# Performance work log

Hardware: AMD Instinct MI355X
Metric: run time of the kernel (lower is better)

## Reference

```python
import jax, jax.numpy as jnp
import numpy as np

N = 100000
E = 1600000
F_IN = 16
HEADS = 4
OUT_CH = 32  # conv_filters[i] // heads = 128 // 4
HID = HEADS * OUT_CH  # 128
N_GRAPHS = 64
N_TARGETS = 4
EPS_BN = 1e-5


def setup_inputs() -> dict:
    key = jax.random.key(0)
    ks = jax.random.split(key, 32)
    glorot = lambda k, shp: jax.random.normal(k, shp, jnp.float32) * np.sqrt(2.0 / (shp[0] + shp[-1]))
    inp = {
        "node_features": jax.random.normal(ks[0], (N, F_IN), jnp.float32),
        "edge_index": jax.random.randint(ks[1], (2, E), 0, N, jnp.int64),
        "batch": jnp.sort(jax.random.randint(ks[2], (N,), 0, N_GRAPHS, jnp.int64)),
        # GAT layer 1: F_IN -> HEADS*OUT_CH
        "W1": glorot(ks[3], (F_IN, HID)),
        "b1": jnp.zeros((HID,), jnp.float32),
        "att_src1": glorot(ks[4], (HEADS, OUT_CH)),
        "att_dst1": glorot(ks[5], (HEADS, OUT_CH)),
        "bn_g1": jnp.ones((HID,), jnp.float32),
        "bn_b1": jnp.zeros((HID,), jnp.float32),
        # GAT layer 2: HID -> HID
        "W2": glorot(ks[6], (HID, HID)),
        "b2": jnp.zeros((HID,), jnp.float32),
        "att_src2": glorot(ks[7], (HEADS, OUT_CH)),
        "att_dst2": glorot(ks[8], (HEADS, OUT_CH)),
        "bn_g2": jnp.ones((HID,), jnp.float32),
        "bn_b2": jnp.zeros((HID,), jnp.float32),
        # dense head 128 -> 64 -> 32 -> 4
        "d1_W": glorot(ks[9], (HID, HID // 2)),
        "d1_b": jnp.zeros((HID // 2,), jnp.float32),
        "bn_g_d1": jnp.ones((HID // 2,), jnp.float32),
        "bn_b_d1": jnp.zeros((HID // 2,), jnp.float32),
        "d2_W": glorot(ks[10], (HID // 2, HID // 4)),
        "d2_b": jnp.zeros((HID // 4,), jnp.float32),
        "bn_g_d2": jnp.ones((HID // 4,), jnp.float32),
        "bn_b_d2": jnp.zeros((HID // 4,), jnp.float32),
        "fc_W": glorot(ks[11], (HID // 4, N_TARGETS)),
        "fc_b": jnp.zeros((N_TARGETS,), jnp.float32),
    }
    return inp


def batch_norm(x, gamma, beta):
    # training-mode BatchNorm1d: biased batch stats over dim 0
    mu = jnp.mean(x, axis=0)
    var = jnp.mean(jnp.square(x - mu), axis=0)
    return gamma * (x - mu) * jax.lax.rsqrt(var + EPS_BN) + beta


def gat_conv(x, src, dst, W, b, att_src, att_dst):
    # PyG GATConv (shared lin, concat heads): h = x @ W -> [N, H, C]
    h = (x @ W).reshape(-1, HEADS, OUT_CH)
    a_s = jnp.sum(h * att_src, axis=-1)  # [N, H]
    a_d = jnp.sum(h * att_dst, axis=-1)  # [N, H]
    e = jax.nn.leaky_relu(a_s[src] + a_d[dst], 0.2)  # [E, H]
    # softmax over incoming edges per destination node
    m = jax.ops.segment_max(e, dst, num_segments=N)
    m = jnp.where(jnp.isfinite(m), m, 0.0)
    w = jnp.exp(e - m[dst])
    s = jax.ops.segment_sum(w, dst, num_segments=N)
    alpha = w / (s[dst] + 1e-16)  # [E, H]
    out = jax.ops.segment_sum(h[src] * alpha[:, :, None], dst, num_segments=N)
    return out.reshape(-1, HID) + b


def reference(node_features, edge_index, batch,
              W1, b1, att_src1, att_dst1, bn_g1, bn_b1,
              W2, b2, att_src2, att_dst2, bn_g2, bn_b2,
              d1_W, d1_b, bn_g_d1, bn_b_d1,
              d2_W, d2_b, bn_g_d2, bn_b_d2,
              fc_W, fc_b):
    src, dst = edge_index[0], edge_index[1]
    x = gat_conv(node_features, src, dst, W1, b1, att_src1, att_dst1)
    x = jax.nn.relu(batch_norm(x, bn_g1, bn_b1))
    x = gat_conv(x, src, dst, W2, b2, att_src2, att_dst2)
    x = jax.nn.relu(batch_norm(x, bn_g2, bn_b2))
    # global mean pool over graphs
    sums = jax.ops.segment_sum(x, batch, num_segments=N_GRAPHS)
    cnt = jax.ops.segment_sum(jnp.ones((x.shape[0],), x.dtype), batch, num_segments=N_GRAPHS)
    g = sums / jnp.maximum(cnt, 1.0)[:, None]  # [G, HID]
    g = jax.nn.relu(batch_norm(g @ d1_W + d1_b, bn_g_d1, bn_b_d1))
    g = jax.nn.relu(batch_norm(g @ d2_W + d2_b, bn_g_d2, bn_b_d2))
    return g @ fc_W + fc_b
```

## Files before the change

kernel.cpp:

```cpp
#include <hip/hip_runtime.h>

#define HID 128
#define NG 64

__device__ __forceinline__ float lrelu(float v) { return v > 0.0f ? v : 0.2f * v; }

__device__ __forceinline__ unsigned int bf16rne(float f) {
    unsigned int u = __float_as_uint(f);
    return (u + 0x7fffu + ((u >> 16) & 1u)) >> 16;
}
__device__ __forceinline__ unsigned int packbf(float a, float b) {
    return bf16rne(a) | (bf16rne(b) << 16);
}

template <int K, bool BN>
__global__ __launch_bounds__(256) void k_gemm(const float* __restrict__ xin,
        const float* __restrict__ W,
        const float* __restrict__ scale, const float* __restrict__ shift,
        const float* __restrict__ attS, const float* __restrict__ attD,
        unsigned short* __restrict__ h, float* __restrict__ as_, float* __restrict__ ad_, int N)
{
    __shared__ float xs[64][K];
    constexpr int K4 = K / 4;
    int t = threadIdx.x;
    int cq = t & 31;
    int nr = t >> 5;

    float4 atS = ((const float4*)attS)[cq];
    float4 atD = ((const float4*)attD)[cq];

    for (int n0 = blockIdx.x * 64; n0 < N; n0 += gridDim.x * 64) {
        int nrem = N - n0; if (nrem > 64) nrem = 64;
        for (int idx = t; idx < 64 * K4; idx += 256) {
            int n = idx / K4, k4 = idx % K4;
            float4 v = make_float4(0.f, 0.f, 0.f, 0.f);
            if (n < nrem) {
                v = ((const float4*)(xin + (size_t)(n0 + n) * K))[k4];
                if (BN) {
                    float4 sc = ((const float4*)scale)[k4];
                    float4 sh = ((const float4*)shift)[k4];
                    v.x = fmaf(v.x, sc.x, sh.x); v.x = v.x > 0.f ? v.x : 0.f;
                    v.y = fmaf(v.y, sc.y, sh.y); v.y = v.y > 0.f ? v.y : 0.f;
                    v.z = fmaf(v.z, sc.z, sh.z); v.z = v.z > 0.f ? v.z : 0.f;
                    v.w = fmaf(v.w, sc.w, sh.w); v.w = v.w > 0.f ? v.w : 0.f;
                }
            }
            *(float4*)(&xs[n][k4 * 4]) = v;
        }
        __syncthreads();

        float4 acc[8];
#pragma unroll
        for (int j = 0; j < 8; ++j) acc[j] = make_float4(0.f, 0.f, 0.f, 0.f);

        const float4* W4 = (const float4*)W;
#pragma unroll 2
        for (int k4 = 0; k4 < K4; ++k4) {
            float4 w0 = W4[(k4 * 4 + 0) * 32 + cq];
            float4 w1 = W4[(k4 * 4 + 1) * 32 + cq];
            float4 w2 = W4[(k4 * 4 + 2) * 32 + cq];
            float4 w3 = W4[(k4 * 4 + 3) * 32 + cq];
#pragma unroll
            for (int j = 0; j < 8; ++j) {
                float4 xv = *(const float4*)(&xs[nr * 8 + j][k4 * 4]);
                acc[j].x = fmaf(xv.x, w0.x, acc[j].x);
                acc[j].y = fmaf(xv.x, w0.y, acc[j].y);
                acc[j].z = fmaf(xv.x, w0.z, acc[j].z);
                acc[j].w = fmaf(xv.x, w0.w, acc[j].w);
                acc[j].x = fmaf(xv.y, w1.x, acc[j].x);
                acc[j].y = fmaf(xv.y, w1.y, acc[j].y);
                acc[j].z = fmaf(xv.y, w1.z, acc[j].z);
                acc[j].w = fmaf(xv.y, w1.w, acc[j].w);
                acc[j].x = fmaf(xv.z, w2.x, acc[j].x);
                acc[j].y = fmaf(xv.z, w2.y, acc[j].y);
                acc[j].z = fmaf(xv.z, w2.z, acc[j].z);
                acc[j].w = fmaf(xv.z, w2.w, acc[j].w);
                acc[j].x = fmaf(xv.w, w3.x, acc[j].x);
                acc[j].y = fmaf(xv.w, w3.y, acc[j].y);
                acc[j].z = fmaf(xv.w, w3.z, acc[j].z);
                acc[j].w = fmaf(xv.w, w3.w, acc[j].w);
            }
        }

#pragma unroll
        for (int j = 0; j < 8; ++j) {
            int n = nr * 8 + j;
            bool ok = (n < nrem);
            if (ok) {
                unsigned int lo = packbf(acc[j].x, acc[j].y);
                unsigned int hi = packbf(acc[j].z, acc[j].w);
                ((uint2*)(h + (size_t)(n0 + n) * 128))[cq] = make_uint2(lo, hi);
            }
            float ps = acc[j].x * atS.x + acc[j].y * atS.y + acc[j].z * atS.z + acc[j].w * atS.w;
            float pd = acc[j].x * atD.x + acc[j].y * atD.y + acc[j].z * atD.z + acc[j].w * atD.w;
            ps += __shfl_xor(ps, 1); pd += __shfl_xor(pd, 1);
            ps += __shfl_xor(ps, 2); pd += __shfl_xor(pd, 2);
            ps += __shfl_xor(ps, 4); pd += __shfl_xor(pd, 4);
            if (ok && (cq & 7) == 0) {
                int hd = cq >> 3;
                as_[(size_t)(n0 + n) * 4 + hd] = ps;
                ad_[(size_t)(n0 + n) * 4 + hd] = pd;
            }
        }
        __syncthreads();
    }
}

__global__ __launch_bounds__(256) void k_bhist(const int* __restrict__ ei,
        int* __restrict__ bSize, int E, int nB)
{
    __shared__ int hist[1024];
    int t = threadIdx.x;
    for (int i = t; i < nB; i += 256) hist[i] = 0;
    __syncthreads();
    int chunk = (E + gridDim.x - 1) / gridDim.x;
    int lo = blockIdx.x * chunk, hi = lo + chunk; if (hi > E) hi = E;
    for (int e = lo + t; e < hi; e += 256) atomicAdd(&hist[ei[E + e] >> 8], 1);
    __syncthreads();
    for (int i = t; i < nB; i += 256) { int c = hist[i]; if (c) atomicAdd(&bSize[i], c); }
}

__global__ __launch_bounds__(512) void k_bscan(const int* __restrict__ bSize,
        int* __restrict__ bOff, int* __restrict__ bCur, int nB)
{
    __shared__ int part[512];
    int t = threadIdx.x;
    part[t] = (t < nB) ? bSize[t] : 0;
    __syncthreads();
    for (int off = 1; off < 512; off <<= 1) {
        int u = (t >= off) ? part[t - off] : 0;
        __syncthreads();
        part[t] += u;
        __syncthreads();
    }
    int ex = (t == 0) ? 0 : part[t - 1];
    if (t < nB) { bOff[t] = ex; bCur[t] = ex; }
    if (t == nB - 1) bOff[nB] = part[t];
}

__global__ __launch_bounds__(256) void k_part(const int* __restrict__ ei,
        int* __restrict__ bCur, unsigned long long* __restrict__ bucketBuf, int E, int nB)
{
    __shared__ int hist[1024];
    __shared__ int base[1024];
    int t = threadIdx.x;
    int chunk = (E + gridDim.x - 1) / gridDim.x;
    int lo = blockIdx.x * chunk, hi = lo + chunk; if (hi > E) hi = E;
    for (int i = t; i < nB; i += 256) hist[i] = 0;
    __syncthreads();
    for (int e = lo + t; e < hi; e += 256) atomicAdd(&hist[ei[E + e] >> 8], 1);
    __syncthreads();
    for (int i = t; i < nB; i += 256) {
        int c = hist[i];
        base[i] = c ? atomicAdd(&bCur[i], c) : 0;
        hist[i] = 0;
    }
    __syncthreads();
    for (int e = lo + t; e < hi; e += 256) {
        int s = ei[e], d = ei[E + e];
        int b = d >> 8;
        int pos = base[b] + atomicAdd(&hist[b], 1);
        bucketBuf[pos] = ((unsigned long long)(unsigned)d << 32) | (unsigned)s;
    }
}

__global__ __launch_bounds__(256) void k_build(const unsigned long long* __restrict__ bucketBuf,
        const int* __restrict__ bOff, int* __restrict__ rowPtr, int* __restrict__ sSrc, int N)
{
    __shared__ int lhist[256];
    __shared__ int sOut[8192];
    int b = blockIdx.x;
    int dlo = b << 8;
    int dhi = dlo + 256; if (dhi > N) dhi = N;
    int base = bOff[b], end = bOff[b + 1];
    int sz = end - base;
    int t = threadIdx.x;
    lhist[t] = 0;
    __syncthreads();
    for (int i = t; i < sz; i += 256) {
        int d = (int)(bucketBuf[base + i] >> 32);
        atomicAdd(&lhist[d - dlo], 1);
    }
    __syncthreads();
    for (int off = 1; off < 256; off <<= 1) {
        int u = (t >= off) ? lhist[t - off] : 0;
        __syncthreads();
        lhist[t] += u;
        __syncthreads();
    }
    int pfx = (t == 0) ? 0 : lhist[t - 1];
    if (dlo + t < dhi) rowPtr[dlo + t] = base + pfx;
    if (t == 0 && dhi == N) rowPtr[N] = end;
    __syncthreads();
    lhist[t] = pfx;
    __syncthreads();
    if (sz <= 8192) {
        for (int i = t; i < sz; i += 256) {
            unsigned long long p = bucketBuf[base + i];
            int d = (int)(p >> 32), s = (int)(p & 0xffffffffu);
            int pos = atomicAdd(&lhist[d - dlo], 1);
            sOut[pos] = s;
        }
        __syncthreads();
        for (int i = t; i < sz; i += 256) sSrc[base + i] = sOut[i];
    } else {
        for (int i = t; i < sz; i += 256) {
            unsigned long long p = bucketBuf[base + i];
            int d = (int)(p >> 32), s = (int)(p & 0xffffffffu);
            int pos = atomicAdd(&lhist[d - dlo], 1);
            sSrc[base + pos] = s;
        }
    }
}

__global__ __launch_bounds__(256) void k_alpha(const int* __restrict__ rowPtr,
        const int* __restrict__ sSrc,
        const float* __restrict__ as_, const float* __restrict__ ad_,
        float* __restrict__ alpha, float* __restrict__ sums, int N)
{
    int t = threadIdx.x;
    int lane8 = t & 7;
    int d = blockIdx.x * 32 + (t >> 3);
    if (d >= N) return;
    int b0 = rowPtr[d], b1 = rowPtr[d + 1];
    float4 adv = ((const float4*)ad_)[d];

    float4 m = make_float4(-3.4e38f, -3.4e38f, -3.4e38f, -3.4e38f);
    for (int j = b0 + lane8; j < b1; j += 8) {
        int s = sSrc[j];
        float4 a = ((const float4*)as_)[s];
        m.x = fmaxf(m.x, lrelu(a.x + adv.x));
        m.y = fmaxf(m.y, lrelu(a.y + adv.y));
        m.z = fmaxf(m.z, lrelu(a.z + adv.z));
        m.w = fmaxf(m.w, lrelu(a.w + adv.w));
    }
#pragma unroll
    for (int off = 1; off < 8; off <<= 1) {
        m.x = fmaxf(m.x, __shfl_xor(m.x, off));
        m.y = fmaxf(m.y, __shfl_xor(m.y, off));
        m.z = fmaxf(m.z, __shfl_xor(m.z, off));
        m.w = fmaxf(m.w, __shfl_xor(m.w, off));
    }
    float4 sum = make_float4(0.f, 0.f, 0.f, 0.f);
    for (int j = b0 + lane8; j < b1; j += 8) {
        int s = sSrc[j];
        float4 a = ((const float4*)as_)[s];
        float4 w;
        w.x = __expf(lrelu(a.x + adv.x) - m.x);
        w.y = __expf(lrelu(a.y + adv.y) - m.y);
        w.z = __expf(lrelu(a.z + adv.z) - m.z);
        w.w = __expf(lrelu(a.w + adv.w) - m.w);
        ((float4*)alpha)[j] = w;
        sum.x += w.x; sum.y += w.y; sum.z += w.z; sum.w += w.w;
    }
#pragma unroll
    for (int off = 1; off < 8; off <<= 1) {
        sum.x += __shfl_xor(sum.x, off);
        sum.y += __shfl_xor(sum.y, off);
        sum.z += __shfl_xor(sum.z, off);
        sum.w += __shfl_xor(sum.w, off);
    }
    if (lane8 == 0) ((float4*)sums)[d] = sum;
}

__global__ __launch_bounds__(256) void k_agg(const int* __restrict__ rowPtr,
        const int* __restrict__ sSrc,
        const float* __restrict__ alpha, const float* __restrict__ sums,
        const unsigned short* __restrict__ h, float* __restrict__ out, int N)
{
    int t = threadIdx.x;
    int lane = t & 31;
    int d = blockIdx.x * 8 + (t >> 5);
    if (d >= N) return;
    int hd = lane >> 3;
    int b0 = rowPtr[d], b1 = rowPtr[d + 1];
    const uint2* h2 = (const uint2*)h;

    float4 acc = make_float4(0.f, 0.f, 0.f, 0.f);
    int j = b0;
    for (; j + 4 <= b1; j += 4) {
        int s0 = sSrc[j], s1 = sSrc[j + 1], s2 = sSrc[j + 2], s3 = sSrc[j + 3];
        float w0 = alpha[(size_t)j * 4 + hd];
        float w1 = alpha[(size_t)(j + 1) * 4 + hd];
        float w2 = alpha[(size_t)(j + 2) * 4 + hd];
        float w3 = alpha[(size_t)(j + 3) * 4 + hd];
        uint2 u0 = h2[(size_t)s0 * 32 + lane];
        uint2 u1 = h2[(size_t)s1 * 32 + lane];
        uint2 u2 = h2[(size_t)s2 * 32 + lane];
        uint2 u3 = h2[(size_t)s3 * 32 + lane];
        acc.x = fmaf(w0, __uint_as_float(u0.x << 16), acc.x);
        acc.y = fmaf(w0, __uint_as_float(u0.x & 0xffff0000u), acc.y);
        acc.z = fmaf(w0, __uint_as_float(u0.y << 16), acc.z);
        acc.w = fmaf(w0, __uint_as_float(u0.y & 0xffff0000u), acc.w);
        acc.x = fmaf(w1, __uint_as_float(u1.x << 16), acc.x);
        acc.y = fmaf(w1, __uint_as_float(u1.x & 0xffff0000u), acc.y);
        acc.z = fmaf(w1, __uint_as_float(u1.y << 16), acc.z);
        acc.w = fmaf(w1, __uint_as_float(u1.y & 0xffff0000u), acc.w);
        acc.x = fmaf(w2, __uint_as_float(u2.x << 16), acc.x);
        acc.y = fmaf(w2, __uint_as_float(u2.x & 0xffff0000u), acc.y);
        acc.z = fmaf(w2, __uint_as_float(u2.y << 16), acc.z);
        acc.w = fmaf(w2, __uint_as_float(u2.y & 0xffff0000u), acc.w);
        acc.x = fmaf(w3, __uint_as_float(u3.x << 16), acc.x);
        acc.y = fmaf(w3, __uint_as_float(u3.x & 0xffff0000u), acc.y);
        acc.z = fmaf(w3, __uint_as_float(u3.y << 16), acc.z);
        acc.w = fmaf(w3, __uint_as_float(u3.y & 0xffff0000u), acc.w);
    }
    for (; j < b1; ++j) {
        int s = sSrc[j];
        float w = alpha[(size_t)j * 4 + hd];
        uint2 u = h2[(size_t)s * 32 + lane];
        acc.x = fmaf(w, __uint_as_float(u.x << 16), acc.x);
        acc.y = fmaf(w, __uint_as_float(u.x & 0xffff0000u), acc.y);
        acc.z = fmaf(w, __uint_as_float(u.y << 16), acc.z);
        acc.w = fmaf(w, __uint_as_float(u.y & 0xffff0000u), acc.w);
    }
    float inv = 1.f / (sums[(size_t)d * 4 + hd] + 1e-16f);
    acc.x *= inv; acc.y *= inv; acc.z *= inv; acc.w *= inv;
    ((float4*)out)[(size_t)d * 32 + lane] = acc;
}

__global__ __launch_bounds__(256) void k_bnstats(const float* __restrict__ x,
        double* __restrict__ sums, int N)
{
    __shared__ float r1[256], r2[256];
    int t = threadIdx.x;
    int c = t & 127;
    int half = t >> 7;
    float s1 = 0.f, s2 = 0.f;
    for (int n = blockIdx.x * 2 + half; n < N; n += gridDim.x * 2) {
        float v = x[(size_t)n * 128 + c];
        s1 += v; s2 += v * v;
    }
    r1[t] = s1; r2[t] = s2;
    __syncthreads();
    if (t < 128) {
        s1 = r1[t] + r1[t + 128];
        s2 = r2[t] + r2[t + 128];
        atomicAdd(&sums[t], (double)s1);
        atomicAdd(&sums[128 + t], (double)s2);
    }
}

__global__ __launch_bounds__(128) void k_bnscale(const double* __restrict__ sums,
        const float* __restrict__ gamma, const float* __restrict__ beta,
        float* __restrict__ scale, float* __restrict__ shift, int N)
{
    int c = threadIdx.x;
    double mu = sums[c] / (double)N;
    double var = sums[128 + c] / (double)N - mu * mu;
    if (var < 0.0) var = 0.0;
    double rs = 1.0 / sqrt(var + 1e-5);
    float sc = (float)((double)gamma[c] * rs);
    scale[c] = sc;
    shift[c] = beta[c] - (float)mu * sc;
}

__global__ __launch_bounds__(128) void k_pool(const float* __restrict__ x,
        const int* __restrict__ batch, const float* __restrict__ scale, const float* __restrict__ shift,
        float* __restrict__ gsum, float* __restrict__ gcnt, int N)
{
    int lane = threadIdx.x & 31;
    int r = threadIdx.x >> 5;
    int n0 = blockIdx.x * 64;
    if (n0 >= N) return;
    int n1 = n0 + 64; if (n1 > N) n1 = N;
    float4 sc = ((const float4*)scale)[lane];
    float4 sh = ((const float4*)shift)[lane];
    float4 acc = make_float4(0.f, 0.f, 0.f, 0.f);
    int cnt = 0, cur = -1;
    for (int n = n0 + r; n < n1; n += 4) {
        int g = batch[n];
        if (g != cur) {
            if (cur >= 0) {
                atomicAdd(&gsum[cur * 128 + lane * 4 + 0], acc.x);
                atomicAdd(&gsum[cur * 128 + lane * 4 + 1], acc.y);
                atomicAdd(&gsum[cur * 128 + lane * 4 + 2], acc.z);
                atomicAdd(&gsum[cur * 128 + lane * 4 + 3], acc.w);
                if (lane == 0) atomicAdd(&gcnt[cur], (float)cnt);
            }
            acc = make_float4(0.f, 0.f, 0.f, 0.f); cnt = 0; cur = g;
        }
        float4 v = ((const float4*)x)[(size_t)n * 32 + lane];
        v.x = fmaf(v.x, sc.x, sh.x); v.x = v.x > 0.f ? v.x : 0.f;
        v.y = fmaf(v.y, sc.y, sh.y); v.y = v.y > 0.f ? v.y : 0.f;
        v.z = fmaf(v.z, sc.z, sh.z); v.z = v.z > 0.f ? v.z : 0.f;
        v.w = fmaf(v.w, sc.w, sh.w); v.w = v.w > 0.f ? v.w : 0.f;
        acc.x += v.x; acc.y += v.y; acc.z += v.z; acc.w += v.w;
        cnt++;
    }
    if (cur >= 0) {
        atomicAdd(&gsum[cur * 128 + lane * 4 + 0], acc.x);
        atomicAdd(&gsum[cur * 128 + lane * 4 + 1], acc.y);
        atomicAdd(&gsum[cur * 128 + lane * 4 + 2], acc.z);
        atomicAdd(&gsum[cur * 128 + lane * 4 + 3], acc.w);
        if (lane == 0) atomicAdd(&gcnt[cur], (float)cnt);
    }
}

__global__ __launch_bounds__(256) void k_head(const float* __restrict__ gsum, const float* __restrict__ gcnt,
        const float* __restrict__ d1W, const float* __restrict__ d1b,
        const float* __restrict__ g_d1, const float* __restrict__ b_d1,
        const float* __restrict__ d2W, const float* __restrict__ d2b,
        const float* __restrict__ g_d2, const float* __restrict__ b_d2,
        const float* __restrict__ fcW, const float* __restrict__ fcb,
        float* __restrict__ out)
{
    __shared__ float G[64 * 128];
    __shared__ float Y1[64 * 64];
    __shared__ float Y2[64 * 32];
    int t = threadIdx.x;
    for (int i = t; i < 64 * 128; i += 256) {
        int g = i >> 7;
        float cv = gcnt[g]; if (cv < 1.f) cv = 1.f;
        G[i] = gsum[i] / cv;
    }
    __syncthreads();
    for (int i = t; i < 64 * 64; i += 256) {
        int r = i >> 6, j = i & 63;
        float a = 0.f;
        for (int k = 0; k < 128; ++k) a = fmaf(G[r * 128 + k], d1W[k * 64 + j], a);
        Y1[i] = a + d1b[j];
    }
    __syncthreads();
    if (t < 64) {
        float s1 = 0.f, s2 = 0.f;
        for (int r = 0; r < 64; ++r) { float v = Y1[r * 64 + t]; s1 += v; s2 += v * v; }
        float mu = s1 / 64.f, var = s2 / 64.f - mu * mu; if (var < 0.f) var = 0.f;
        float rs = 1.0f / sqrtf(var + 1e-5f);
        float scv = g_d1[t] * rs, shv = b_d1[t] - mu * scv;
        for (int r = 0; r < 64; ++r) {
            float v = fmaf(Y1[r * 64 + t], scv, shv);
            Y1[r * 64 + t] = v > 0.f ? v : 0.f;
        }
    }
    __syncthreads();
    for (int i = t; i < 64 * 32; i += 256) {
        int r = i >> 5, j = i & 31;
        float a = 0.f;
        for (int k = 0; k < 64; ++k) a = fmaf(Y1[r * 64 + k], d2W[k * 32 + j], a);
        Y2[i] = a + d2b[j];
    }
    __syncthreads();
    if (t < 32) {
        float s1 = 0.f, s2 = 0.f;
        for (int r = 0; r < 64; ++r) { float v = Y2[r * 32 + t]; s1 += v; s2 += v * v; }
        float mu = s1 / 64.f, var = s2 / 64.f - mu * mu; if (var < 0.f) var = 0.f;
        float rs = 1.0f / sqrtf(var + 1e-5f);
        float scv = g_d2[t] * rs, shv = b_d2[t] - mu * scv;
        for (int r = 0; r < 64; ++r) {
            float v = fmaf(Y2[r * 32 + t], scv, shv);
            Y2[r * 32 + t] = v > 0.f ? v : 0.f;
        }
    }
    __syncthreads();
    {
        int r = t >> 2, j = t & 3;
        float a = 0.f;
        for (int k = 0; k < 32; ++k) a = fmaf(Y2[r * 32 + k], fcW[k * 4 + j], a);
        out[t] = a + fcb[j];
    }
}

extern "C" void kernel_launch(void* const* d_in, const int* in_sizes, int n_in,
                              void* d_out, int out_size, void* d_ws, size_t ws_size,
                              hipStream_t stream) {
    const int N = in_sizes[0] / 16;
    const int E = in_sizes[1] / 2;
    const int nB = (N + 255) >> 8;

    const float* x        = (const float*)d_in[0];
    const int*   ei       = (const int*)d_in[1];
    const int*   batch    = (const int*)d_in[2];
    const float* W1       = (const float*)d_in[3];
    const float* att_s1   = (const float*)d_in[5];
    const float* att_d1   = (const float*)d_in[6];
    const float* bn_g1    = (const float*)d_in[7];
    const float* bn_b1    = (const float*)d_in[8];
    const float* W2       = (const float*)d_in[9];
    const float* att_s2   = (const float*)d_in[11];
    const float* att_d2   = (const float*)d_in[12];
    const float* bn_g2    = (const float*)d_in[13];
    const float* bn_b2    = (const float*)d_in[14];
    const float* d1W      = (const float*)d_in[15];
    const float* d1b      = (const float*)d_in[16];
    const float* g_d1     = (const float*)d_in[17];
    const float* b_d1     = (const float*)d_in[18];
    const float* d2W      = (const float*)d_in[19];
    const float* d2b      = (const float*)d_in[20];
    const float* g_d2     = (const float*)d_in[21];
    const float* b_d2     = (const float*)d_in[22];
    const float* fcW      = (const float*)d_in[23];
    const float* fcb      = (const float*)d_in[24];
    float* out = (float*)d_out;

    float* ws = (float*)d_ws;
    size_t o = 0;
    unsigned short* hbuf = (unsigned short*)(ws + o); o += (size_t)N * 64;
    float* outb   = ws + o;  o += (size_t)N * 128;
    float* as_    = ws + o;  o += (size_t)N * 4;
    float* ad_    = ws + o;  o += (size_t)N * 4;
    float* alpha  = ws + o;  o += (size_t)E * 4;
    float* sums   = ws + o;  o += (size_t)N * 4;
    float* scale1 = ws + o;  o += 128;
    float* shift1 = ws + o;  o += 128;
    float* scale2 = ws + o;  o += 128;
    float* shift2 = ws + o;  o += 128;
    size_t zoff = o;
    double* bnsum = (double*)(ws + o); o += 512;
    float* gsum   = ws + o;  o += 64 * 128;
    float* gcnt   = ws + o;  o += 64;
    int*   bSize  = (int*)(ws + o); o += 1024;
    size_t zbytes = (o - zoff) * 4;
    int* rowPtr   = (int*)(ws + o); o += (size_t)N + 1;
    int* sSrc     = (int*)(ws + o); o += E;
    int* bOff     = (int*)(ws + o); o += 1025;
    int* bCur     = (int*)(ws + o); o += 1024;
    o = (o + 1) & ~(size_t)1;
    unsigned long long* bucketBuf = (unsigned long long*)(ws + o); o += (size_t)E * 2;

    hipMemsetAsync(ws + zoff, 0, zbytes, stream);

    k_bhist<<<256, 256, 0, stream>>>(ei, bSize, E, nB);
    k_bscan<<<1, 512, 0, stream>>>(bSize, bOff, bCur, nB);
    k_part<<<256, 256, 0, stream>>>(ei, bCur, bucketBuf, E, nB);
    k_build<<<nB, 256, 0, stream>>>(bucketBuf, bOff, rowPtr, sSrc, N);

    int gemm_grid = (N + 63) / 64;
    int alpha_grid = (N + 31) / 32;
    int agg_grid = (N + 7) / 8;

    k_gemm<16, false><<<gemm_grid, 256, 0, stream>>>(x, W1, nullptr, nullptr,
            att_s1, att_d1, hbuf, as_, ad_, N);
    k_alpha<<<alpha_grid, 256, 0, stream>>>(rowPtr, sSrc, as_, ad_, alpha, sums, N);
    k_agg<<<agg_grid, 256, 0, stream>>>(rowPtr, sSrc, alpha, sums, hbuf, outb, N);
    k_bnstats<<<1024, 256, 0, stream>>>(outb, bnsum, N);
    k_bnscale<<<1, 128, 0, stream>>>(bnsum, bn_g1, bn_b1, scale1, shift1, N);

    hipMemsetAsync((void*)bnsum, 0, 512 * 4, stream);

    k_gemm<128, true><<<gemm_grid, 256, 0, stream>>>(outb, W2, scale1, shift1,
            att_s2, att_d2, hbuf, as_, ad_, N);
    k_alpha<<<alpha_grid, 256, 0, stream>>>(rowPtr, sSrc, as_, ad_, alpha, sums, N);
    k_agg<<<agg_grid, 256, 0, stream>>>(rowPtr, sSrc, alpha, sums, hbuf, outb, N);
    k_bnstats<<<1024, 256, 0, stream>>>(outb, bnsum, N);
    k_bnscale<<<1, 128, 0, stream>>>(bnsum, bn_g2, bn_b2, scale2, shift2, N);

    k_pool<<<(N + 63) / 64, 128, 0, stream>>>(outb, batch, scale2, shift2, gsum, gcnt, N);
    k_head<<<1, 256, 0, stream>>>(gsum, gcnt, d1W, d1b, g_d1, b_d1,
                                  d2W, d2b, g_d2, b_d2, fcW, fcb, out);
}
```

Measured before the change: 567.1 us.

## Fuse softmax into aggregation, pack bucket entries to 32 bits, drop bnsum memset

Removes the separate k_alpha kernel and the E×4 alpha buffer. k_agg now computes the per-head softmax denominator itself and recomputes the edge weights from as_/ad_ on the fly, with no max subtraction. Bucket entries shrink from 64-bit (dst,src) pairs to 32-bit words holding the dst low byte and a 24-bit src, which halves partition traffic. Two bnsum buffers replace the mid-stream memset. The trade-offs are an extra pass over neighbours to gather as_ for the sums, a risk of exp overflow without the max shift, and a src limit of 2^24.

```diff
diff --git a/kernel.cpp b/kernel.cpp
--- a/kernel.cpp
+++ b/kernel.cpp
@@ -139,7 +139,7 @@
 }
 
 __global__ __launch_bounds__(256) void k_part(const int* __restrict__ ei,
-        int* __restrict__ bCur, unsigned long long* __restrict__ bucketBuf, int E, int nB)
+        int* __restrict__ bCur, unsigned int* __restrict__ bucketBuf, int E, int nB)
 {
     __shared__ int hist[1024];
     __shared__ int base[1024];
@@ -160,11 +160,11 @@
         int s = ei[e], d = ei[E + e];
         int b = d >> 8;
         int pos = base[b] + atomicAdd(&hist[b], 1);
-        bucketBuf[pos] = ((unsigned long long)(unsigned)d << 32) | (unsigned)s;
-    }
-}
-
-__global__ __launch_bounds__(256) void k_build(const unsigned long long* __restrict__ bucketBuf,
+        bucketBuf[pos] = ((unsigned)(d & 255) << 24) | (unsigned)s;
+    }
+}
+
+__global__ __launch_bounds__(256) void k_build(const unsigned int* __restrict__ bucketBuf,
         const int* __restrict__ bOff, int* __restrict__ rowPtr, int* __restrict__ sSrc, int N)
 {
     __shared__ int lhist[256];
@@ -178,8 +178,7 @@
     lhist[t] = 0;
     __syncthreads();
     for (int i = t; i < sz; i += 256) {
-        int d = (int)(bucketBuf[base + i] >> 32);
-        atomicAdd(&lhist[d - dlo], 1);
+        atomicAdd(&lhist[bucketBuf[base + i] >> 24], 1);
     }
     __syncthreads();
     for (int off = 1; off < 256; off <<= 1) {
@@ -196,76 +195,24 @@
     __syncthreads();
     if (sz <= 8192) {
         for (int i = t; i < sz; i += 256) {
-            unsigned long long p = bucketBuf[base + i];
-            int d = (int)(p >> 32), s = (int)(p & 0xffffffffu);
-            int pos = atomicAdd(&lhist[d - dlo], 1);
-            sOut[pos] = s;
+            unsigned int p = bucketBuf[base + i];
+            int pos = atomicAdd(&lhist[p >> 24], 1);
+            sOut[pos] = (int)(p & 0xffffffu);
         }
         __syncthreads();
         for (int i = t; i < sz; i += 256) sSrc[base + i] = sOut[i];
     } else {
         for (int i = t; i < sz; i += 256) {
-            unsigned long long p = bucketBuf[base + i];
-            int d = (int)(p >> 32), s = (int)(p & 0xffffffffu);
-            int pos = atomicAdd(&lhist[d - dlo], 1);
-            sSrc[base + pos] = s;
-        }
-    }
-}
-
-__global__ __launch_bounds__(256) void k_alpha(const int* __restrict__ rowPtr,
+            unsigned int p = bucketBuf[base + i];
+            int pos = atomicAdd(&lhist[p >> 24], 1);
+            sSrc[base + pos] = (int)(p & 0xffffffu);
+        }
+    }
+}
+
+__global__ __launch_bounds__(256) void k_agg(const int* __restrict__ rowPtr,
         const int* __restrict__ sSrc,
         const float* __restrict__ as_, const float* __restrict__ ad_,
-        float* __restrict__ alpha, float* __restrict__ sums, int N)
-{
-    int t = threadIdx.x;
-    int lane8 = t & 7;
-    int d = blockIdx.x * 32 + (t >> 3);
-    if (d >= N) return;
-    int b0 = rowPtr[d], b1 = rowPtr[d + 1];
-    float4 adv = ((const float4*)ad_)[d];
-
-    float4 m = make_float4(-3.4e38f, -3.4e38f, -3.4e38f, -3.4e38f);
-    for (int j = b0 + lane8; j < b1; j += 8) {
-        int s = sSrc[j];
-        float4 a = ((const float4*)as_)[s];
-        m.x = fmaxf(m.x, lrelu(a.x + adv.x));
-        m.y = fmaxf(m.y, lrelu(a.y + adv.y));
-        m.z = fmaxf(m.z, lrelu(a.z + adv.z));
-        m.w = fmaxf(m.w, lrelu(a.w + adv.w));
-    }
-#pragma unroll
-    for (int off = 1; off < 8; off <<= 1) {
-        m.x = fmaxf(m.x, __shfl_xor(m.x, off));
-        m.y = fmaxf(m.y, __shfl_xor(m.y, off));
-        m.z = fmaxf(m.z, __shfl_xor(m.z, off));
-        m.w = fmaxf(m.w, __shfl_xor(m.w, off));
-    }
-    float4 sum = make_float4(0.f, 0.f, 0.f, 0.f);
-    for (int j = b0 + lane8; j < b1; j += 8) {
-        int s = sSrc[j];
-        float4 a = ((const float4*)as_)[s];
-        float4 w;
-        w.x = __expf(lrelu(a.x + adv.x) - m.x);
-        w.y = __expf(lrelu(a.y + adv.y) - m.y);
-        w.z = __expf(lrelu(a.z + adv.z) - m.z);
-        w.w = __expf(lrelu(a.w + adv.w) - m.w);
-        ((float4*)alpha)[j] = w;
-        sum.x += w.x; sum.y += w.y; sum.z += w.z; sum.w += w.w;
-    }
-#pragma unroll
-    for (int off = 1; off < 8; off <<= 1) {
-        sum.x += __shfl_xor(sum.x, off);
-        sum.y += __shfl_xor(sum.y, off);
-        sum.z += __shfl_xor(sum.z, off);
-        sum.w += __shfl_xor(sum.w, off);
-    }
-    if (lane8 == 0) ((float4*)sums)[d] = sum;
-}
-
-__global__ __launch_bounds__(256) void k_agg(const int* __restrict__ rowPtr,
-        const int* __restrict__ sSrc,
-        const float* __restrict__ alpha, const float* __restrict__ sums,
         const unsigned short* __restrict__ h, float* __restrict__ out, int N)
 {
     int t = threadIdx.x;
@@ -274,16 +221,37 @@
     if (d >= N) return;
     int hd = lane >> 3;
     int b0 = rowPtr[d], b1 = rowPtr[d + 1];
+    float4 adv = ((const float4*)ad_)[d];
+
+    float4 sm = make_float4(0.f, 0.f, 0.f, 0.f);
+    for (int j = b0 + lane; j < b1; j += 32) {
+        int s = sSrc[j];
+        float4 a = ((const float4*)as_)[s];
+        sm.x += __expf(lrelu(a.x + adv.x));
+        sm.y += __expf(lrelu(a.y + adv.y));
+        sm.z += __expf(lrelu(a.z + adv.z));
+        sm.w += __expf(lrelu(a.w + adv.w));
+    }
+#pragma unroll
+    for (int off = 1; off < 32; off <<= 1) {
+        sm.x += __shfl_xor(sm.x, off);
+        sm.y += __shfl_xor(sm.y, off);
+        sm.z += __shfl_xor(sm.z, off);
+        sm.w += __shfl_xor(sm.w, off);
+    }
+    float sumh = (hd == 0) ? sm.x : (hd == 1) ? sm.y : (hd == 2) ? sm.z : sm.w;
+    float inv = 1.f / (sumh + 1e-16f);
+    float advh = (hd == 0) ? adv.x : (hd == 1) ? adv.y : (hd == 2) ? adv.z : adv.w;
+
     const uint2* h2 = (const uint2*)h;
-
     float4 acc = make_float4(0.f, 0.f, 0.f, 0.f);
     int j = b0;
     for (; j + 4 <= b1; j += 4) {
         int s0 = sSrc[j], s1 = sSrc[j + 1], s2 = sSrc[j + 2], s3 = sSrc[j + 3];
-        float w0 = alpha[(size_t)j * 4 + hd];
-        float w1 = alpha[(size_t)(j + 1) * 4 + hd];
-        float w2 = alpha[(size_t)(j + 2) * 4 + hd];
-        float w3 = alpha[(size_t)(j + 3) * 4 + hd];
+        float w0 = __expf(lrelu(as_[(size_t)s0 * 4 + hd] + advh));
+        float w1 = __expf(lrelu(as_[(size_t)s1 * 4 + hd] + advh));
+        float w2 = __expf(lrelu(as_[(size_t)s2 * 4 + hd] + advh));
+        float w3 = __expf(lrelu(as_[(size_t)s3 * 4 + hd] + advh));
         uint2 u0 = h2[(size_t)s0 * 32 + lane];
         uint2 u1 = h2[(size_t)s1 * 32 + lane];
         uint2 u2 = h2[(size_t)s2 * 32 + lane];
@@ -307,14 +275,13 @@
     }
     for (; j < b1; ++j) {
         int s = sSrc[j];
-        float w = alpha[(size_t)j * 4 + hd];
+        float w = __expf(lrelu(as_[(size_t)s * 4 + hd] + advh));
         uint2 u = h2[(size_t)s * 32 + lane];
         acc.x = fmaf(w, __uint_as_float(u.x << 16), acc.x);
         acc.y = fmaf(w, __uint_as_float(u.x & 0xffff0000u), acc.y);
         acc.z = fmaf(w, __uint_as_float(u.y << 16), acc.z);
         acc.w = fmaf(w, __uint_as_float(u.y & 0xffff0000u), acc.w);
     }
-    float inv = 1.f / (sums[(size_t)d * 4 + hd] + 1e-16f);
     acc.x *= inv; acc.y *= inv; acc.z *= inv; acc.w *= inv;
     ((float4*)out)[(size_t)d * 32 + lane] = acc;
 }
@@ -499,14 +466,13 @@
     float* outb   = ws + o;  o += (size_t)N * 128;
     float* as_    = ws + o;  o += (size_t)N * 4;
     float* ad_    = ws + o;  o += (size_t)N * 4;
-    float* alpha  = ws + o;  o += (size_t)E * 4;
-    float* sums   = ws + o;  o += (size_t)N * 4;
     float* scale1 = ws + o;  o += 128;
     float* shift1 = ws + o;  o += 128;
     float* scale2 = ws + o;  o += 128;
     float* shift2 = ws + o;  o += 128;
     size_t zoff = o;
-    double* bnsum = (double*)(ws + o); o += 512;
+    double* bnsumA = (double*)(ws + o); o += 512;
+    double* bnsumB = (double*)(ws + o); o += 512;
     float* gsum   = ws + o;  o += 64 * 128;
     float* gcnt   = ws + o;  o += 64;
     int*   bSize  = (int*)(ws + o); o += 1024;
@@ -515,8 +481,7 @@
     int* sSrc     = (int*)(ws + o); o += E;
     int* bOff     = (int*)(ws + o); o += 1025;
     int* bCur     = (int*)(ws + o); o += 1024;
-    o = (o + 1) & ~(size_t)1;
-    unsigned long long* bucketBuf = (unsigned long long*)(ws + o); o += (size_t)E * 2;
+    unsigned int* bucketBuf = (unsigned int*)(ws + o); o += E;
 
     hipMemsetAsync(ws + zoff, 0, zbytes, stream);
 
@@ -526,24 +491,19 @@
     k_build<<<nB, 256, 0, stream>>>(bucketBuf, bOff, rowPtr, sSrc, N);
 
     int gemm_grid = (N + 63) / 64;
-    int alpha_grid = (N + 31) / 32;
     int agg_grid = (N + 7) / 8;
 
     k_gemm<16, false><<<gemm_grid, 256, 0, stream>>>(x, W1, nullptr, nullptr,
             att_s1, att_d1, hbuf, as_, ad_, N);
-    k_alpha<<<alpha_grid, 256, 0, stream>>>(rowPtr, sSrc, as_, ad_, alpha, sums, N);
-    k_agg<<<agg_grid, 256, 0, stream>>>(rowPtr, sSrc, alpha, sums, hbuf, outb, N);
-    k_bnstats<<<1024, 256, 0, stream>>>(outb, bnsum, N);
-    k_bnscale<<<1, 128, 0, stream>>>(bnsum, bn_g1, bn_b1, scale1, shift1, N);
-
-    hipMemsetAsync((void*)bnsum, 0, 512 * 4, stream);
+    k_agg<<<agg_grid, 256, 0, stream>>>(rowPtr, sSrc, as_, ad_, hbuf, outb, N);
+    k_bnstats<<<1024, 256, 0, stream>>>(outb, bnsumA, N);
+    k_bnscale<<<1, 128, 0, stream>>>(bnsumA, bn_g1, bn_b1, scale1, shift1, N);
 
     k_gemm<128, true><<<gemm_grid, 256, 0, stream>>>(outb, W2, scale1, shift1,
             att_s2, att_d2, hbuf, as_, ad_, N);
-    k_alpha<<<alpha_grid, 256, 0, stream>>>(rowPtr, sSrc, as_, ad_, alpha, sums, N);
-    k_agg<<<agg_grid, 256, 0, stream>>>(rowPtr, sSrc, alpha, sums, hbuf, outb, N);
-    k_bnstats<<<1024, 256, 0, stream>>>(outb, bnsum, N);
-    k_bnscale<<<1, 128, 0, stream>>>(bnsum, bn_g2, bn_b2, scale2, shift2, N);
+    k_agg<<<agg_grid, 256, 0, stream>>>(rowPtr, sSrc, as_, ad_, hbuf, outb, N);
+    k_bnstats<<<1024, 256, 0, stream>>>(outb, bnsumB, N);
+    k_bnscale<<<1, 128, 0, stream>>>(bnsumB, bn_g2, bn_b2, scale2, shift2, N);
 
     k_pool<<<(N + 63) / 64, 128, 0, stream>>>(outb, batch, scale2, shift2, gsum, gcnt, N);
     k_head<<<1, 256, 0, stream>>>(gsum, gcnt, d1W, d1b, g_d1, b_d1,
```

New measurement: 540.8 us. -4.6%, faster.
